# Kernel tuning notes

Measured on AMD Instinct MI355X. Metric: run time of the kernel, lower is better.

Reference implementation:

```python
import jax, jax.numpy as jnp
import numpy as np

N_HEADS = 16
D_MODEL = 1024
D_K = D_MODEL // N_HEADS
NEG_INF = -1e9


def setup_inputs() -> dict:
    key = jax.random.key(0)
    ks = jax.random.split(key, 7)
    B, S, D = 4, 2048, D_MODEL
    scale = 1.0 / np.sqrt(D)
    return {
        "query": jax.random.normal(ks[0], (B, S, D), dtype=jnp.float32),
        "key": jax.random.normal(ks[1], (B, S, D), dtype=jnp.float32),
        "value": jax.random.normal(ks[2], (B, S, D), dtype=jnp.float32),
        "Wq": jax.random.normal(ks[3], (D, D), dtype=jnp.float32) * scale,
        "Wk": jax.random.normal(ks[4], (D, D), dtype=jnp.float32) * scale,
        "Wv": jax.random.normal(ks[5], (D, D), dtype=jnp.float32) * scale,
        "Wo": jax.random.normal(ks[6], (D, D), dtype=jnp.float32) * scale,
    }


def _split_heads(x):
    # (B, S, D) -> (B, H, S, d_k)
    B, S, _ = x.shape
    return x.reshape(B, S, N_HEADS, D_K).transpose(0, 2, 1, 3)


def reference(query, key, value, Wq, Wk, Wv, Wo):
    B, S, D = query.shape
    # nn.Linear(d, d, bias=False): y = x @ W.T ; here W is stored as [out, in]
    Q = _split_heads(query @ Wq.T)
    K = _split_heads(key @ Wk.T)
    V = _split_heads(value @ Wv.T)
    scores = jnp.einsum("bhqd,bhkd->bhqk", Q, K) / jnp.sqrt(jnp.float32(D_K))
    # causal mask: 0 on/below diagonal, -1e9 above
    causal = jnp.where(
        jnp.tril(jnp.ones((S, S), dtype=bool)), 0.0, NEG_INF
    ).astype(scores.dtype)
    scores = scores + causal[None, None, :, :]
    attn = jax.nn.softmax(scores, axis=-1)
    heads = jnp.einsum("bhqk,bhkd->bhqd", attn, V)
    concat = heads.transpose(0, 2, 1, 3).reshape(B, S, D)
    out = concat @ Wo.T
    return out  # dropout p=0.0 -> identity
```

## Files before the change

kernel.cpp:

```cpp
#include <hip/hip_runtime.h>
#include <hip/hip_bf16.h>

typedef short short8 __attribute__((ext_vector_type(8)));
typedef short short4v __attribute__((ext_vector_type(4)));
typedef float floatx4 __attribute__((ext_vector_type(4)));

constexpr int BATCH = 4;
constexpr int SEQ = 2048;
constexpr int DMODEL = 1024;
constexpr int NHEADS = 16;
constexpr int DKH = 64;
constexpr int MROWS = BATCH * SEQ;
constexpr size_t NE = (size_t)MROWS * DMODEL;
constexpr size_t WE = (size_t)DMODEL * DMODEL;
constexpr float SC = 0.18033688011112042f;

__device__ __forceinline__ short f2bf(float f) {
    unsigned u = __float_as_uint(f);
    u += 0x7fffu + ((u >> 16) & 1u);
    return (short)(u >> 16);
}

__device__ __forceinline__ short2 pk2(float a, float b) {
    __hip_bfloat162 h = __float22bfloat162_rn(float2{a, b});
    short2 r;
    __builtin_memcpy(&r, &h, 4);
    return r;
}

__device__ __forceinline__ void ld16(const void* g, void* l) {
    __builtin_amdgcn_global_load_lds(
        (const __attribute__((address_space(1))) unsigned int*)g,
        (__attribute__((address_space(3))) unsigned int*)l, 16, 0, 0);
}

__device__ __forceinline__ void sync_vm3() {
    asm volatile("s_waitcnt vmcnt(3)" ::: "memory");
    __builtin_amdgcn_sched_barrier(0);
    __builtin_amdgcn_s_barrier();
    __builtin_amdgcn_sched_barrier(0);
}
__device__ __forceinline__ void sync_vm0() {
    asm volatile("s_waitcnt vmcnt(0)" ::: "memory");
    __builtin_amdgcn_sched_barrier(0);
    __builtin_amdgcn_s_barrier();
    __builtin_amdgcn_sched_barrier(0);
}

__global__ __launch_bounds__(256) void f32_to_bf16(const float* __restrict__ s,
                                                   short* __restrict__ d, int n4) {
    int i = blockIdx.x * blockDim.x + threadIdx.x;
    const int stride = gridDim.x * blockDim.x;
    for (; i < n4; i += stride) {
        float4 f = ((const float4*)s)[i];
        short4v v;
        v[0] = f2bf(f.x); v[1] = f2bf(f.y); v[2] = f2bf(f.z); v[3] = f2bf(f.w);
        ((short4v*)d)[i] = v;
    }
}

__global__ __launch_bounds__(256) void cvt2(const float* __restrict__ s0,
                                            const float* __restrict__ s1,
                                            short* __restrict__ d0,
                                            short* __restrict__ d1, int n4) {
    const float* s = blockIdx.y ? s1 : s0;
    short* d = blockIdx.y ? d1 : d0;
    int i = blockIdx.x * blockDim.x + threadIdx.x;
    const int stride = gridDim.x * blockDim.x;
    for (; i < n4; i += stride) {
        float4 f = ((const float4*)s)[i];
        short4v v;
        v[0] = f2bf(f.x); v[1] = f2bf(f.y); v[2] = f2bf(f.z); v[3] = f2bf(f.w);
        ((short4v*)d)[i] = v;
    }
}

__global__ __launch_bounds__(256) void wcvt3(const float* __restrict__ a,
                                             const float* __restrict__ b,
                                             const float* __restrict__ c,
                                             short* __restrict__ dst, int n4) {
    const float* s = (blockIdx.y == 0) ? a : (blockIdx.y == 1) ? b : c;
    const float m = (blockIdx.y == 0) ? SC : 1.0f;
    short* d = dst + (size_t)blockIdx.y * (size_t)n4 * 4;
    int i = blockIdx.x * blockDim.x + threadIdx.x;
    const int stride = gridDim.x * blockDim.x;
    for (; i < n4; i += stride) {
        float4 f = ((const float4*)s)[i];
        short4v v;
        v[0] = f2bf(f.x * m); v[1] = f2bf(f.y * m);
        v[2] = f2bf(f.z * m); v[3] = f2bf(f.w * m);
        ((short4v*)d)[i] = v;
    }
}

template <int KS>
__device__ __forceinline__ void do_phase(const short* Ab, const short* Bb,
                                         floatx4 (&acc)[4][4], int wm, int wn,
                                         int lane16, int quad, int fsw) {
    short8 af[4], bf[4];
#pragma unroll
    for (int i = 0; i < 4; ++i)
        af[i] = *(const short8*)&Ab[KS * (256 * 32) + (wm + i * 16 + lane16) * 32 +
                                    ((quad ^ fsw) * 8)];
#pragma unroll
    for (int j = 0; j < 4; ++j)
        bf[j] = *(const short8*)&Bb[KS * (128 * 32) + (wn + j * 16 + lane16) * 32 +
                                    ((quad ^ fsw) * 8)];
    __builtin_amdgcn_s_setprio(1);
#pragma unroll
    for (int i = 0; i < 4; ++i)
#pragma unroll
        for (int j = 0; j < 4; ++j)
            acc[i][j] = __builtin_amdgcn_mfma_f32_16x16x32_bf16(af[i], bf[j],
                                                                acc[i][j], 0, 0, 0);
    __builtin_amdgcn_s_setprio(0);
}

template <int OUT_MODE>
__device__ __forceinline__ void gemm_body(const short* A, const short* B,
                                          void* Yp) {
    __shared__ __align__(16) short Asw[2][2][256 * 32];
    __shared__ __align__(16) short Bsw[2][2][128 * 32];

    const int tid = threadIdx.x;
    const int w = tid >> 6, l = tid & 63;
    const int lane16 = l & 15, quad = l >> 4;
    const int wm = (w >> 1) * 64, wn = (w & 1) * 64;
    const int m0 = blockIdx.x * 256, n0 = blockIdx.y * 128;
    const int fsw = (lane16 >> 1) & 3;

    const int rr = tid >> 2;
    const int cc = (tid & 3) ^ ((rr >> 1) & 3);
    const int ldsW0 = (w * 16) * 32;
    const int ldsW1 = (128 + w * 16) * 32;

    auto stA = [&](int k0, int bufi, int ks) {
        const short* g = A + (size_t)(m0 + rr) * DMODEL + k0 + ks * 32 + cc * 8;
        ld16(g, &Asw[bufi][ks][ldsW0]);
        ld16(g + (size_t)128 * DMODEL, &Asw[bufi][ks][ldsW1]);
    };
    auto stB = [&](int k0, int bufi, int ks) {
        const short* g = B + (size_t)(n0 + rr) * DMODEL + k0 + ks * 32 + cc * 8;
        ld16(g, &Bsw[bufi][ks][ldsW0]);
    };

    floatx4 acc[4][4];
#pragma unroll
    for (int i = 0; i < 4; ++i)
#pragma unroll
        for (int j = 0; j < 4; ++j) acc[i][j] = {0.f, 0.f, 0.f, 0.f};

    constexpr int NT = DMODEL / 64;
    stA(0, 0, 0); stB(0, 0, 0);
    stA(0, 0, 1); stB(0, 0, 1);
    sync_vm3();

    for (int t = 0; t < NT; ++t) {
        const int cur = t & 1, nxt = cur ^ 1;
        const short* Ab = &Asw[cur][0][0];
        const short* Bb = &Bsw[cur][0][0];
        const int k1 = (t + 1) * 64;
        const bool more = (t + 1 < NT);

        if (more) { stA(k1, nxt, 0); stB(k1, nxt, 0); }
        do_phase<0>(Ab, Bb, acc, wm, wn, lane16, quad, fsw);
        if (more) sync_vm3(); else sync_vm0();
        if (more) { stA(k1, nxt, 1); stB(k1, nxt, 1); }
        do_phase<1>(Ab, Bb, acc, wm, wn, lane16, quad, fsw);
        if (more) sync_vm3();
    }

    const int gmb = m0 + wm, gnb = n0 + wn;
    if (OUT_MODE == 0) {
        short* Y = (short*)Yp;
#pragma unroll
        for (int mi = 0; mi < 4; ++mi)
#pragma unroll
            for (int ni = 0; ni < 4; ++ni) {
                const int gm = gmb + mi * 16 + quad * 4;
                const int gn = gnb + ni * 16 + lane16;
#pragma unroll
                for (int r = 0; r < 4; ++r)
                    Y[(size_t)(gm + r) * DMODEL + gn] = f2bf(acc[mi][ni][r]);
            }
    } else if (OUT_MODE == 1) {
        short* Y = (short*)Yp;
#pragma unroll
        for (int mi = 0; mi < 4; ++mi)
#pragma unroll
            for (int ni = 0; ni < 4; ++ni) {
                const int gm = gmb + mi * 16 + quad * 4;
                const int gn = gnb + ni * 16 + lane16;
                const int bb = gm >> 11, ss = gm & (SEQ - 1);
                const int hh = gn >> 6, dd = gn & 63;
                const size_t base = ((size_t)(bb * NHEADS + hh) * DKH + dd) * SEQ + ss;
                short4v vv;
#pragma unroll
                for (int r = 0; r < 4; ++r) vv[r] = f2bf(acc[mi][ni][r]);
                *(short4v*)(Y + base) = vv;
            }
    } else {
        float* Y = (float*)Yp;
#pragma unroll
        for (int mi = 0; mi < 4; ++mi)
#pragma unroll
            for (int ni = 0; ni < 4; ++ni) {
                const int gm = gmb + mi * 16 + quad * 4;
                const int gn = gnb + ni * 16 + lane16;
#pragma unroll
                for (int r = 0; r < 4; ++r)
                    Y[(size_t)(gm + r) * DMODEL + gn] = acc[mi][ni][r];
            }
    }
}

template <int OUT_MODE>
__global__ __launch_bounds__(512, 2) void gemm_nt(const short* __restrict__ A,
                                                  const short* __restrict__ B,
                                                  void* __restrict__ Yp) {
    gemm_body<OUT_MODE>(A, B, Yp);
}

__global__ __launch_bounds__(512, 2) void gemm_qk(const short* __restrict__ Aq,
                                                  const short* __restrict__ Ak,
                                                  const short* __restrict__ Wqk,
                                                  short* __restrict__ Yq,
                                                  short* __restrict__ Yk) {
    const int z = blockIdx.z;
    gemm_body<0>(z ? Ak : Aq, Wqk + (size_t)z * WE, z ? Yk : Yq);
}

__global__ __launch_bounds__(256, 4) void attn_fwd(const short* __restrict__ Qb,
                                                   const short* __restrict__ Kb,
                                                   const short* __restrict__ Vt,
                                                   short* __restrict__ Oc) {
    __shared__ __align__(16) short Kl[2][64 * 64];
    __shared__ __align__(16) short Vl[2][64 * 64];
    __shared__ __align__(16) short Plds[4][16][64];

    const int bh = blockIdx.x;
    const int qt = (int)(gridDim.y - 1) - blockIdx.y;
    const int b = bh >> 4, h = bh & 15;
    const int tid = threadIdx.x;
    const int w = tid >> 6, l = tid & 63;
    const int lane16 = l & 15, quad = l >> 4;

    const short* Qrow =
        Qb + ((size_t)b * SEQ + qt * 64 + w * 16 + lane16) * DMODEL + h * DKH;
    const short8 qf0 = *(const short8*)(Qrow + quad * 8);
    const short8 qf1 = *(const short8*)(Qrow + 32 + quad * 8);

    const int r0 = tid >> 3, c0 = tid & 7;
    const int sc0 = c0 ^ (r0 & 7);
    const short* Kg = Kb + (size_t)b * SEQ * DMODEL + h * DKH;
    const short* Vg = Vt + (size_t)bh * DKH * SEQ;

    short8 kra, krb, vra, vrb;
    kra = *(const short8*)(Kg + (size_t)r0 * DMODEL + c0 * 8);
    krb = *(const short8*)(Kg + (size_t)(r0 + 32) * DMODEL + c0 * 8);
    vra = *(const short8*)(Vg + (size_t)r0 * SEQ + c0 * 8);
    vrb = *(const short8*)(Vg + (size_t)(r0 + 32) * SEQ + c0 * 8);
    *(short8*)&Kl[0][r0 * 64 + sc0 * 8] = kra;
    *(short8*)&Kl[0][(r0 + 32) * 64 + sc0 * 8] = krb;
    *(short8*)&Vl[0][r0 * 64 + sc0 * 8] = vra;
    *(short8*)&Vl[0][(r0 + 32) * 64 + sc0 * 8] = vrb;
    if (qt > 0) {
        kra = *(const short8*)(Kg + (size_t)(64 + r0) * DMODEL + c0 * 8);
        krb = *(const short8*)(Kg + (size_t)(64 + r0 + 32) * DMODEL + c0 * 8);
        vra = *(const short8*)(Vg + (size_t)r0 * SEQ + 64 + c0 * 8);
        vrb = *(const short8*)(Vg + (size_t)(r0 + 32) * SEQ + 64 + c0 * 8);
    }

    floatx4 oacc[4];
#pragma unroll
    for (int ni = 0; ni < 4; ++ni) oacc[ni] = {0.f, 0.f, 0.f, 0.f};
    float Lp = 0.f;
    const int swz = lane16 & 7;
    const int psw = lane16 & 7;

    for (int kt = 0; kt <= qt; ++kt) {
        const int cur = kt & 1;
        __syncthreads();
        if (kt < qt) {
            const int nb = cur ^ 1;
            *(short8*)&Kl[nb][r0 * 64 + sc0 * 8] = kra;
            *(short8*)&Kl[nb][(r0 + 32) * 64 + sc0 * 8] = krb;
            *(short8*)&Vl[nb][r0 * 64 + sc0 * 8] = vra;
            *(short8*)&Vl[nb][(r0 + 32) * 64 + sc0 * 8] = vrb;
            if (kt + 1 < qt) {
                const int kn = (kt + 2) * 64;
                kra = *(const short8*)(Kg + (size_t)(kn + r0) * DMODEL + c0 * 8);
                krb = *(const short8*)(Kg + (size_t)(kn + r0 + 32) * DMODEL + c0 * 8);
                vra = *(const short8*)(Vg + (size_t)r0 * SEQ + kn + c0 * 8);
                vrb = *(const short8*)(Vg + (size_t)(r0 + 32) * SEQ + kn + c0 * 8);
            }
        }

        float p[4][4];
#pragma unroll
        for (int nt = 0; nt < 4; ++nt) {
            const short* kr = &Kl[cur][(nt * 16 + lane16) * 64];
            floatx4 st = {0.f, 0.f, 0.f, 0.f};
            st = __builtin_amdgcn_mfma_f32_16x16x32_bf16(
                *(const short8*)(kr + (quad ^ swz) * 8), qf0, st, 0, 0, 0);
            st = __builtin_amdgcn_mfma_f32_16x16x32_bf16(
                *(const short8*)(kr + ((4 + quad) ^ swz) * 8), qf1, st, 0, 0, 0);
#pragma unroll
            for (int r = 0; r < 4; ++r) p[nt][r] = st[r];
        }

#pragma unroll
        for (int nt = 0; nt < 4; ++nt)
#pragma unroll
            for (int r = 0; r < 4; ++r) p[nt][r] = __builtin_amdgcn_exp2f(p[nt][r]);

        if (kt == qt) {
            const int qloc = w * 16 + lane16;
#pragma unroll
            for (int nt = 0; nt < 4; ++nt)
#pragma unroll
                for (int r = 0; r < 4; ++r)
                    if (nt * 16 + quad * 4 + r > qloc) p[nt][r] = 0.f;
        }

        float rs01 = 0.f, rs23 = 0.f;
#pragma unroll
        for (int nt = 0; nt < 4; ++nt)
#pragma unroll
            for (int r = 0; r < 4; ++r) {
                if (nt < 2) rs01 += p[nt][r]; else rs23 += p[nt][r];
            }
        Lp += rs01 + rs23;

#pragma unroll
        for (int nt = 0; nt < 4; ++nt) {
            const short2 lo = pk2(p[nt][0], p[nt][1]);
            const short2 hi = pk2(p[nt][2], p[nt][3]);
            short4v pk;
            pk[0] = lo.x; pk[1] = lo.y; pk[2] = hi.x; pk[3] = hi.y;
            const int pch = (nt * 2 + (quad >> 1)) ^ psw;
            *(short4v*)&Plds[w][lane16][pch * 8 + (quad & 1) * 4] = pk;
        }
        const short8 pf0 = *(const short8*)&Plds[w][lane16][(quad ^ psw) * 8];
        const short8 pf1 = *(const short8*)&Plds[w][lane16][((4 + quad) ^ psw) * 8];

#pragma unroll
        for (int ni = 0; ni < 4; ++ni) {
            const short* vr = &Vl[cur][(ni * 16 + lane16) * 64];
            oacc[ni] = __builtin_amdgcn_mfma_f32_16x16x32_bf16(
                pf0, *(const short8*)(vr + (quad ^ swz) * 8), oacc[ni], 0, 0, 0);
            oacc[ni] = __builtin_amdgcn_mfma_f32_16x16x32_bf16(
                pf1, *(const short8*)(vr + ((4 + quad) ^ swz) * 8), oacc[ni], 0, 0, 0);
        }
    }

    float L = Lp + __shfl_xor(Lp, 16);
    L += __shfl_xor(L, 32);
    float linv[4];
#pragma unroll
    for (int r = 0; r < 4; ++r) linv[r] = 1.f / __shfl(L, quad * 4 + r);
#pragma unroll
    for (int r = 0; r < 4; ++r) {
        const int qg = qt * 64 + w * 16 + quad * 4 + r;
#pragma unroll
        for (int ni = 0; ni < 4; ++ni)
            Oc[((size_t)b * SEQ + qg) * DMODEL + h * DKH + ni * 16 + lane16] =
                f2bf(oacc[ni][r] * linv[r]);
    }
}

extern "C" void kernel_launch(void* const* d_in, const int* in_sizes, int n_in,
                              void* d_out, int out_size, void* d_ws, size_t ws_size,
                              hipStream_t stream) {
    const float* q = (const float*)d_in[0];
    const float* k = (const float*)d_in[1];
    const float* v = (const float*)d_in[2];
    const float* Wq = (const float*)d_in[3];
    const float* Wk = (const float*)d_in[4];
    const float* Wv = (const float*)d_in[5];
    const float* Wo = (const float*)d_in[6];

    short* Qb = (short*)d_ws;
    short* Kb = Qb + NE;
    short* Vt = Kb + NE;
    short* Cc = Vt + NE;
    short* Wqb = (short*)d_out;
    short* Wkb = Wqb + WE;
    short* Wvb = Wqb + 2 * WE;
    short* Kbf = Wqb + 3 * WE;
    short* Wob = Vt;

    dim3 gg(MROWS / 256, DMODEL / 128);
    dim3 gqk(MROWS / 256, DMODEL / 128, 2);
    dim3 ga(BATCH * NHEADS, SEQ / 64);
    const int actN4 = (int)(NE / 4), wN4 = (int)(WE / 4);

    wcvt3<<<dim3(256, 3), 256, 0, stream>>>(Wq, Wk, Wv, (short*)d_out, wN4);
    cvt2<<<dim3(1024, 2), 256, 0, stream>>>(q, k, Cc, Kbf, actN4);
    gemm_qk<<<gqk, 512, 0, stream>>>(Cc, Kbf, Wqb, Qb, Kb);
    f32_to_bf16<<<2048, 256, 0, stream>>>(v, Cc, actN4);
    gemm_nt<1><<<gg, 512, 0, stream>>>(Cc, Wvb, Vt);
    attn_fwd<<<ga, 256, 0, stream>>>(Qb, Kb, Vt, Cc);
    f32_to_bf16<<<512, 256, 0, stream>>>(Wo, Wob, wN4);
    gemm_nt<2><<<gg, 512, 0, stream>>>(Cc, Wob, d_out);
}
```

Measured before the change: 329.0 us.

## Triple-buffer GEMM LDS staging to prefetch two k-tiles ahead

Replaces the double-buffered, half-tile-interleaved GEMM load schedule with a three-stage LDS ring that prefetches tile t+2 while computing tile t. It uses one barrier per k-tile instead of two and waits with vmcnt(6), so a full tile of loads stays in flight. The cost is 1.5x the LDS footprint (about 144KB), which may lower occupancy to one block per CU.

```diff
diff --git a/kernel.cpp b/kernel.cpp
--- a/kernel.cpp
+++ b/kernel.cpp
@@ -34,8 +34,8 @@
         (__attribute__((address_space(3))) unsigned int*)l, 16, 0, 0);
 }
 
-__device__ __forceinline__ void sync_vm3() {
-    asm volatile("s_waitcnt vmcnt(3)" ::: "memory");
+__device__ __forceinline__ void sync_vm6() {
+    asm volatile("s_waitcnt vmcnt(6)" ::: "memory");
     __builtin_amdgcn_sched_barrier(0);
     __builtin_amdgcn_s_barrier();
     __builtin_amdgcn_sched_barrier(0);
@@ -119,8 +119,8 @@
 template <int OUT_MODE>
 __device__ __forceinline__ void gemm_body(const short* A, const short* B,
                                           void* Yp) {
-    __shared__ __align__(16) short Asw[2][2][256 * 32];
-    __shared__ __align__(16) short Bsw[2][2][128 * 32];
+    __shared__ __align__(16) short Asw[3][2][256 * 32];
+    __shared__ __align__(16) short Bsw[3][2][128 * 32];
 
     const int tid = threadIdx.x;
     const int w = tid >> 6, l = tid & 63;
@@ -134,15 +134,17 @@
     const int ldsW0 = (w * 16) * 32;
     const int ldsW1 = (128 + w * 16) * 32;
 
-    auto stA = [&](int k0, int bufi, int ks) {
-        const short* g = A + (size_t)(m0 + rr) * DMODEL + k0 + ks * 32 + cc * 8;
-        ld16(g, &Asw[bufi][ks][ldsW0]);
-        ld16(g + (size_t)128 * DMODEL, &Asw[bufi][ks][ldsW1]);
+    auto stage = [&](int t) {
+        const int k0 = t * 64, bufi = t % 3;
+#pragma unroll
+        for (int ks = 0; ks < 2; ++ks) {
+            const short* ga = A + (size_t)(m0 + rr) * DMODEL + k0 + ks * 32 + cc * 8;
+            ld16(ga, &Asw[bufi][ks][ldsW0]);
+            ld16(ga + (size_t)128 * DMODEL, &Asw[bufi][ks][ldsW1]);
+            const short* gb = B + (size_t)(n0 + rr) * DMODEL + k0 + ks * 32 + cc * 8;
+            ld16(gb, &Bsw[bufi][ks][ldsW0]);
+        }
     };
-    auto stB = [&](int k0, int bufi, int ks) {
-        const short* g = B + (size_t)(n0 + rr) * DMODEL + k0 + ks * 32 + cc * 8;
-        ld16(g, &Bsw[bufi][ks][ldsW0]);
-    };
 
     floatx4 acc[4][4];
 #pragma unroll
@@ -151,23 +153,16 @@
         for (int j = 0; j < 4; ++j) acc[i][j] = {0.f, 0.f, 0.f, 0.f};
 
     constexpr int NT = DMODEL / 64;
-    stA(0, 0, 0); stB(0, 0, 0);
-    stA(0, 0, 1); stB(0, 0, 1);
-    sync_vm3();
+    stage(0);
+    stage(1);
 
     for (int t = 0; t < NT; ++t) {
-        const int cur = t & 1, nxt = cur ^ 1;
-        const short* Ab = &Asw[cur][0][0];
-        const short* Bb = &Bsw[cur][0][0];
-        const int k1 = (t + 1) * 64;
-        const bool more = (t + 1 < NT);
-
-        if (more) { stA(k1, nxt, 0); stB(k1, nxt, 0); }
+        if (t + 1 < NT) sync_vm6(); else sync_vm0();
+        if (t + 2 < NT) stage(t + 2);
+        const short* Ab = &Asw[t % 3][0][0];
+        const short* Bb = &Bsw[t % 3][0][0];
         do_phase<0>(Ab, Bb, acc, wm, wn, lane16, quad, fsw);
-        if (more) sync_vm3(); else sync_vm0();
-        if (more) { stA(k1, nxt, 1); stB(k1, nxt, 1); }
         do_phase<1>(Ab, Bb, acc, wm, wn, lane16, quad, fsw);
-        if (more) sync_vm3();
     }
 
     const int gmb = m0 + wm, gnb = n0 + wn;
```

Result: faster. 321.5 us (-2.3%).
